# Kernel optimization log

Measured on AMD Instinct MI355X. Metric: run time of the kernel, lower is better.

## Reference

```python
import jax, jax.numpy as jnp
import numpy as np

NUM_CLASSES = 8
NUM_MAPS = 4
FEAT_C = 2048  # ResNet-50 layer4 channels
HW = 14        # spatial size (448/32)


def setup_inputs() -> dict:
    key = jax.random.key(0)
    k1, k2, k3, k4, k5 = jax.random.split(key, 5)
    B = 64
    x = jax.random.normal(k1, (B, FEAT_C, HW, HW), dtype=jnp.float32)
    down_w = jax.random.normal(k2, (NUM_CLASSES * NUM_MAPS, FEAT_C), dtype=jnp.float32) * 0.02
    down_b = jax.random.normal(k3, (NUM_CLASSES * NUM_MAPS,), dtype=jnp.float32) * 0.02
    fc_w = jax.random.normal(k4, (NUM_CLASSES, 2 * FEAT_C), dtype=jnp.float32) * 0.02
    fc_b = jax.random.normal(k5, (NUM_CLASSES,), dtype=jnp.float32) * 0.02
    return {"x": x, "down_w": down_w, "down_b": down_b, "fc_w": fc_w, "fc_b": fc_b}


def reference(x, down_w, down_b, fc_w, fc_b):
    B = x.shape[0]
    x_ori = x  # [B, 2048, 14, 14] (ResNet features output)
    # downconv: 1x1 conv 2048 -> num_classes*num_maps
    xc = jnp.einsum('bchw,oc->bohw', x_ori, down_w) + down_b[None, :, None, None]  # [B,32,14,14]
    # GMP over full 14x14 window -> [B, 32]
    gmp = jnp.max(xc, axis=(2, 3))
    # spatial_pooling = ClassWisePool(num_maps): mean over groups of num_maps channels
    scores = gmp.reshape(B, NUM_CLASSES, NUM_MAPS).mean(axis=2)  # [B, 8]
    x_out = jax.nn.log_softmax(scores, axis=1)  # first output
    # class-wise pool on the full conv map: [B,32,14,14] -> [B,8,14,14]
    xcp = xc.reshape(B, NUM_CLASSES, NUM_MAPS, HW, HW).mean(axis=2)
    # modulate each class map by its (log-softmax) score
    xcp = xcp * x_out[:, :, None, None]
    # spatial_pooling2 = ClassWisePool(num_classes): mean over 8 class channels -> [B,1,14,14]
    sal = xcp.mean(axis=1, keepdims=True)
    prod = sal * x_ori  # [B,2048,14,14] via broadcast (fused, no copies)
    cat = jnp.concatenate([x_ori, prod], axis=1)  # [B,4096,14,14]
    # GAP 14x14 -> [B,4096]
    gap = cat.mean(axis=(2, 3))
    logits2 = gap @ fc_w.T + fc_b  # [B,8]
    x_conv_out = jax.nn.log_softmax(logits2, axis=1)
    return (x_out, x_conv_out)
```

## Files before the change

kernel.cpp:

```cpp
#include <hip/hip_runtime.h>

#define NCLS 8
#define NMAPS 4
#define NCH 2048
#define HW 196
#define NB 64
#define NOUT 48
#define PF 8

__global__ void build_wct(const float* __restrict__ down_w,
                          const float* __restrict__ fc_w,
                          float* __restrict__ wct) {
    int i = blockIdx.x * 256 + threadIdx.x;
    if (i >= NCH * NOUT) return;
    int c = i / NOUT, o = i % NOUT;
    float v;
    if (o < 32)      v = down_w[o * NCH + c];
    else if (o < 40) v = fc_w[(o - 32) * (2 * NCH) + NCH + c];
    else             v = fc_w[(o - 40) * (2 * NCH) + c];
    wct[c * NOUT + o] = v;
}

__global__ __launch_bounds__(256) void conv48(const float* __restrict__ x,
                                              const float* __restrict__ wct,
                                              float* __restrict__ part,
                                              int cpc, int nchunk) {
    const int b = blockIdx.y;
    const int chunk = blockIdx.x;
    const int p = threadIdx.x;
    const int pp = (p < HW) ? p : (HW - 1);

    float acc[NOUT];
#pragma unroll
    for (int o = 0; o < NOUT; ++o) acc[o] = 0.f;

    const float* xb = x + ((size_t)b * NCH + (size_t)chunk * cpc) * HW + pp;
    const float* wb = wct + (size_t)chunk * cpc * NOUT;

    float xv[PF];
#pragma unroll
    for (int i = 0; i < PF; ++i) xv[i] = xb[i * HW];

    int c0 = 0;
    for (; c0 + 2 * PF <= cpc; c0 += PF) {
        float xn[PF];
#pragma unroll
        for (int i = 0; i < PF; ++i) xn[i] = xb[(c0 + PF + i) * HW];
#pragma unroll
        for (int i = 0; i < PF; ++i) {
            const float* w = wb + (c0 + i) * NOUT;
#pragma unroll
            for (int o = 0; o < NOUT; ++o)
                acc[o] = fmaf(w[o], xv[i], acc[o]);
        }
#pragma unroll
        for (int i = 0; i < PF; ++i) xv[i] = xn[i];
        __asm__ volatile("" ::: "memory");
    }
#pragma unroll
    for (int i = 0; i < PF; ++i) {
        const float* w = wb + (c0 + i) * NOUT;
#pragma unroll
        for (int o = 0; o < NOUT; ++o)
            acc[o] = fmaf(w[o], xv[i], acc[o]);
    }

    if (p < HW) {
        float* dst = part + ((size_t)(b * nchunk + chunk) * NOUT) * HW + p;
#pragma unroll
        for (int o = 0; o < NOUT; ++o) dst[o * HW] = acc[o];
    }
}

__global__ __launch_bounds__(256) void reduce_part(const float* __restrict__ part,
                                                   float* __restrict__ T,
                                                   int nchunk) {
    int idx = blockIdx.x * 256 + threadIdx.x;
    if (idx >= NB * NOUT * HW) return;
    int b = idx / (NOUT * HW);
    int rem = idx - b * NOUT * HW;
    const float* src = part + (size_t)b * nchunk * NOUT * HW + rem;
    float s = 0.f;
    for (int ch = 0; ch < nchunk; ++ch)
        s += src[(size_t)ch * NOUT * HW];
    T[idx] = s;
}

__global__ __launch_bounds__(256) void finish(const float* __restrict__ T,
                                              const float* __restrict__ down_b,
                                              const float* __restrict__ fc_b,
                                              float* __restrict__ out) {
    const int b = blockIdx.x;
    const int tid = threadIdx.x;
    __shared__ float Ts[NOUT * HW];
    __shared__ float gmpS[32];
    __shared__ float scoreS[8];
    __shared__ float xoS[8];
    __shared__ float salS[HW];
    __shared__ float logitS[8];

    {
        const float4* src = (const float4*)(T + (size_t)b * NOUT * HW);
        float4* dst = (float4*)Ts;
        for (int i = tid; i < NOUT * HW / 4; i += 256) dst[i] = src[i];
    }
    __syncthreads();

    if (tid < 32) {
        float m = -1e30f;
        for (int p = 0; p < HW; ++p) m = fmaxf(m, Ts[tid * HW + p]);
        gmpS[tid] = m + down_b[tid];
    }
    __syncthreads();

    if (tid < 8)
        scoreS[tid] = 0.25f * (gmpS[4 * tid] + gmpS[4 * tid + 1] +
                               gmpS[4 * tid + 2] + gmpS[4 * tid + 3]);
    __syncthreads();

    if (tid < 8) {
        float m = -1e30f;
        for (int k = 0; k < 8; ++k) m = fmaxf(m, scoreS[k]);
        float se = 0.f;
        for (int k = 0; k < 8; ++k) se += expf(scoreS[k] - m);
        float xo = scoreS[tid] - m - logf(se);
        xoS[tid] = xo;
        out[b * 8 + tid] = xo;
    }
    __syncthreads();

    if (tid < HW) {
        float s = 0.f;
#pragma unroll
        for (int k = 0; k < 8; ++k) {
            float bs = down_b[4 * k] + down_b[4 * k + 1] +
                       down_b[4 * k + 2] + down_b[4 * k + 3];
            float rs = Ts[(4 * k) * HW + tid] + Ts[(4 * k + 1) * HW + tid] +
                       Ts[(4 * k + 2) * HW + tid] + Ts[(4 * k + 3) * HW + tid] + bs;
            s += xoS[k] * rs;
        }
        salS[tid] = s * (1.f / 32.f);
    }
    __syncthreads();

    if (tid < 8) {
        float t1 = 0.f, t2 = 0.f;
        for (int p = 0; p < HW; ++p) {
            t1 += Ts[(40 + tid) * HW + p];
            t2 += salS[p] * Ts[(32 + tid) * HW + p];
        }
        logitS[tid] = (t1 + t2) * (1.f / 196.f) + fc_b[tid];
    }
    __syncthreads();

    if (tid < 8) {
        float m = -1e30f;
        for (int k = 0; k < 8; ++k) m = fmaxf(m, logitS[k]);
        float se = 0.f;
        for (int k = 0; k < 8; ++k) se += expf(logitS[k] - m);
        out[NB * 8 + b * 8 + tid] = logitS[tid] - m - logf(se);
    }
}

extern "C" void kernel_launch(void* const* d_in, const int* in_sizes, int n_in,
                              void* d_out, int out_size, void* d_ws, size_t ws_size,
                              hipStream_t stream) {
    const float* x      = (const float*)d_in[0];
    const float* down_w = (const float*)d_in[1];
    const float* down_b = (const float*)d_in[2];
    const float* fc_w   = (const float*)d_in[3];
    const float* fc_b   = (const float*)d_in[4];
    float* out = (float*)d_out;

    float* wct  = (float*)d_ws;
    float* T    = wct + NCH * NOUT;
    float* part = T + NB * NOUT * HW;

    size_t base_bytes = ((size_t)NCH * NOUT + (size_t)NB * NOUT * HW) * 4;
    int nchunk = 16;
    if (ws_size < base_bytes + (size_t)NB * 16 * NOUT * HW * 4) nchunk = 8;
    int cpc = NCH / nchunk;

    build_wct<<<(NCH * NOUT + 255) / 256, 256, 0, stream>>>(down_w, fc_w, wct);
    conv48<<<dim3(nchunk, NB), 256, 0, stream>>>(x, wct, part, cpc, nchunk);
    reduce_part<<<(NB * NOUT * HW + 255) / 256, 256, 0, stream>>>(part, T, nchunk);
    finish<<<NB, 256, 0, stream>>>(T, down_b, fc_b, out);
}
```

Before: 205.1 us.

## Split conv outputs into three groups and fold partial reduction into finish

The conv kernel now computes 16 of the 48 output channels per block, with three blocks per channel chunk, cutting accumulator registers to allow more waves per CU. The number of channel chunks drops from 16 to 8, and the separate reduce_part kernel is removed: finish sums the per-chunk partials itself while loading into shared memory. build_wct remaps threads so reads of the source weights are contiguous. In exchange, each x slice is read three times, relying on cache reuse between the sibling blocks that run close together.

```diff
diff --git a/kernel.cpp b/kernel.cpp
--- a/kernel.cpp
+++ b/kernel.cpp
@@ -6,6 +6,8 @@
 #define HW 196
 #define NB 64
 #define NOUT 48
+#define OG 3
+#define OPG 16
 #define PF 8
 
 __global__ void build_wct(const float* __restrict__ down_w,
@@ -13,7 +15,8 @@
                           float* __restrict__ wct) {
     int i = blockIdx.x * 256 + threadIdx.x;
     if (i >= NCH * NOUT) return;
-    int c = i / NOUT, o = i % NOUT;
+    int o = i >> 11;
+    int c = i & (NCH - 1);
     float v;
     if (o < 32)      v = down_w[o * NCH + c];
     else if (o < 40) v = fc_w[(o - 32) * (2 * NCH) + NCH + c];
@@ -26,16 +29,17 @@
                                               float* __restrict__ part,
                                               int cpc, int nchunk) {
     const int b = blockIdx.y;
-    const int chunk = blockIdx.x;
+    const int chunk = blockIdx.x / OG;
+    const int og = blockIdx.x - chunk * OG;
     const int p = threadIdx.x;
     const int pp = (p < HW) ? p : (HW - 1);
 
-    float acc[NOUT];
+    float acc[OPG];
 #pragma unroll
-    for (int o = 0; o < NOUT; ++o) acc[o] = 0.f;
+    for (int o = 0; o < OPG; ++o) acc[o] = 0.f;
 
     const float* xb = x + ((size_t)b * NCH + (size_t)chunk * cpc) * HW + pp;
-    const float* wb = wct + (size_t)chunk * cpc * NOUT;
+    const float* wb = wct + (size_t)chunk * cpc * NOUT + og * OPG;
 
     float xv[PF];
 #pragma unroll
@@ -50,7 +54,7 @@
         for (int i = 0; i < PF; ++i) {
             const float* w = wb + (c0 + i) * NOUT;
 #pragma unroll
-            for (int o = 0; o < NOUT; ++o)
+            for (int o = 0; o < OPG; ++o)
                 acc[o] = fmaf(w[o], xv[i], acc[o]);
         }
 #pragma unroll
@@ -61,35 +65,22 @@
     for (int i = 0; i < PF; ++i) {
         const float* w = wb + (c0 + i) * NOUT;
 #pragma unroll
-        for (int o = 0; o < NOUT; ++o)
+        for (int o = 0; o < OPG; ++o)
             acc[o] = fmaf(w[o], xv[i], acc[o]);
     }
 
     if (p < HW) {
-        float* dst = part + ((size_t)(b * nchunk + chunk) * NOUT) * HW + p;
+        float* dst = part + ((size_t)(b * nchunk + chunk) * NOUT + og * OPG) * HW + p;
 #pragma unroll
-        for (int o = 0; o < NOUT; ++o) dst[o * HW] = acc[o];
+        for (int o = 0; o < OPG; ++o) dst[o * HW] = acc[o];
     }
 }
 
-__global__ __launch_bounds__(256) void reduce_part(const float* __restrict__ part,
-                                                   float* __restrict__ T,
-                                                   int nchunk) {
-    int idx = blockIdx.x * 256 + threadIdx.x;
-    if (idx >= NB * NOUT * HW) return;
-    int b = idx / (NOUT * HW);
-    int rem = idx - b * NOUT * HW;
-    const float* src = part + (size_t)b * nchunk * NOUT * HW + rem;
-    float s = 0.f;
-    for (int ch = 0; ch < nchunk; ++ch)
-        s += src[(size_t)ch * NOUT * HW];
-    T[idx] = s;
-}
-
-__global__ __launch_bounds__(256) void finish(const float* __restrict__ T,
+__global__ __launch_bounds__(256) void finish(const float* __restrict__ part,
                                               const float* __restrict__ down_b,
                                               const float* __restrict__ fc_b,
-                                              float* __restrict__ out) {
+                                              float* __restrict__ out,
+                                              int nchunk) {
     const int b = blockIdx.x;
     const int tid = threadIdx.x;
     __shared__ float Ts[NOUT * HW];
@@ -100,9 +91,17 @@
     __shared__ float logitS[8];
 
     {
-        const float4* src = (const float4*)(T + (size_t)b * NOUT * HW);
+        const float4* src = (const float4*)(part + (size_t)b * nchunk * NOUT * HW);
         float4* dst = (float4*)Ts;
-        for (int i = tid; i < NOUT * HW / 4; i += 256) dst[i] = src[i];
+        const int n4 = NOUT * HW / 4;
+        for (int i = tid; i < n4; i += 256) {
+            float4 s = src[i];
+            for (int ch = 1; ch < nchunk; ++ch) {
+                float4 v = src[(size_t)ch * n4 + i];
+                s.x += v.x; s.y += v.y; s.z += v.z; s.w += v.w;
+            }
+            dst[i] = s;
+        }
     }
     __syncthreads();
 
@@ -173,16 +172,14 @@
     float* out = (float*)d_out;
 
     float* wct  = (float*)d_ws;
-    float* T    = wct + NCH * NOUT;
-    float* part = T + NB * NOUT * HW;
+    float* part = wct + NCH * NOUT;
 
-    size_t base_bytes = ((size_t)NCH * NOUT + (size_t)NB * NOUT * HW) * 4;
-    int nchunk = 16;
-    if (ws_size < base_bytes + (size_t)NB * 16 * NOUT * HW * 4) nchunk = 8;
+    size_t base_bytes = (size_t)NCH * NOUT * 4;
+    int nchunk = 8;
+    if (ws_size < base_bytes + (size_t)NB * 8 * NOUT * HW * 4) nchunk = 4;
     int cpc = NCH / nchunk;
 
     build_wct<<<(NCH * NOUT + 255) / 256, 256, 0, stream>>>(down_w, fc_w, wct);
-    conv48<<<dim3(nchunk, NB), 256, 0, stream>>>(x, wct, part, cpc, nchunk);
-    reduce_part<<<(NB * NOUT * HW + 255) / 256, 256, 0, stream>>>(part, T, nchunk);
-    finish<<<NB, 256, 0, stream>>>(T, down_b, fc_b, out);
+    conv48<<<dim3(nchunk * OG, NB), 256, 0, stream>>>(x, wct, part, cpc, nchunk);
+    finish<<<NB, 256, 0, stream>>>(part, down_b, fc_b, out, nchunk);
 }
```

After: 202.6 us. About the same (-1.2%).

## Replace FP32 FMA channel conv with bf16 MFMA 16x16x32 kernel

Applied to the files above, without the earlier changes.

The 1x1 conv plus the fused fc projections, a 48-output GEMM over 2048 channels, now runs on bf16 matrix cores instead of scalar FP32 FMAs. Weights are pre-packed into MFMA A-fragment layout in bf16. Each wave converts strided x loads to bf16 on the fly and issues three MFMAs per 16-pixel tile. This cuts ALU work but lowers precision to bf16 inputs. The chunk count is fixed at 16, removing the workspace-size fallback.

```diff
diff --git a/kernel.cpp b/kernel.cpp
--- a/kernel.cpp
+++ b/kernel.cpp
@@ -1,87 +1,120 @@
 #include <hip/hip_runtime.h>
 
-#define NCLS 8
-#define NMAPS 4
 #define NCH 2048
 #define HW 196
 #define NB 64
 #define NOUT 48
-#define PF 8
-
-__global__ void build_wct(const float* __restrict__ down_w,
-                          const float* __restrict__ fc_w,
-                          float* __restrict__ wct) {
-    int i = blockIdx.x * 256 + threadIdx.x;
-    if (i >= NCH * NOUT) return;
-    int c = i / NOUT, o = i % NOUT;
-    float v;
-    if (o < 32)      v = down_w[o * NCH + c];
-    else if (o < 40) v = fc_w[(o - 32) * (2 * NCH) + NCH + c];
-    else             v = fc_w[(o - 40) * (2 * NCH) + c];
-    wct[c * NOUT + o] = v;
-}
-
-__global__ __launch_bounds__(256) void conv48(const float* __restrict__ x,
-                                              const float* __restrict__ wct,
-                                              float* __restrict__ part,
-                                              int cpc, int nchunk) {
+#define NCHUNK 16
+#define CPC (NCH / NCHUNK)
+#define KSTEPS (CPC / 32)
+#define KGTOT (NCH / 32)
+#define NT 13
+#define MT 3
+
+typedef __attribute__((ext_vector_type(8))) short bf16x8;
+typedef __attribute__((ext_vector_type(4))) float f32x4;
+
+__device__ __forceinline__ short f2bf(float f) {
+    unsigned int u = __float_as_uint(f);
+    u = u + 0x7fffu + ((u >> 16) & 1u);
+    return (short)(u >> 16);
+}
+
+__global__ void build_afrag(const float* __restrict__ down_w,
+                            const float* __restrict__ fc_w,
+                            bf16x8* __restrict__ afrag) {
+    int t = blockIdx.x * 256 + threadIdx.x;
+    if (t >= KGTOT * MT * 64) return;
+    int lane = t & 63;
+    int frag = t >> 6;
+    int mt = frag % MT;
+    int kg = frag / MT;
+    int o = mt * 16 + (lane & 15);
+    int cbase = kg * 32 + (lane >> 4) * 8;
+    bf16x8 v;
+#pragma unroll
+    for (int j = 0; j < 8; ++j) {
+        int c = cbase + j;
+        float w;
+        if (o < 32)      w = down_w[o * NCH + c];
+        else if (o < 40) w = fc_w[(o - 32) * (2 * NCH) + NCH + c];
+        else             w = fc_w[(o - 40) * (2 * NCH) + c];
+        v[j] = f2bf(w);
+    }
+    afrag[frag * 64 + lane] = v;
+}
+
+__global__ __launch_bounds__(256, 4) void conv_mfma(const float* __restrict__ x,
+                                                    const bf16x8* __restrict__ afrag,
+                                                    float* __restrict__ part) {
+    const int chunk = blockIdx.x;
     const int b = blockIdx.y;
-    const int chunk = blockIdx.x;
-    const int p = threadIdx.x;
-    const int pp = (p < HW) ? p : (HW - 1);
-
-    float acc[NOUT];
-#pragma unroll
-    for (int o = 0; o < NOUT; ++o) acc[o] = 0.f;
-
-    const float* xb = x + ((size_t)b * NCH + (size_t)chunk * cpc) * HW + pp;
-    const float* wb = wct + (size_t)chunk * cpc * NOUT;
-
-    float xv[PF];
-#pragma unroll
-    for (int i = 0; i < PF; ++i) xv[i] = xb[i * HW];
-
-    int c0 = 0;
-    for (; c0 + 2 * PF <= cpc; c0 += PF) {
-        float xn[PF];
-#pragma unroll
-        for (int i = 0; i < PF; ++i) xn[i] = xb[(c0 + PF + i) * HW];
-#pragma unroll
-        for (int i = 0; i < PF; ++i) {
-            const float* w = wb + (c0 + i) * NOUT;
-#pragma unroll
-            for (int o = 0; o < NOUT; ++o)
-                acc[o] = fmaf(w[o], xv[i], acc[o]);
-        }
-#pragma unroll
-        for (int i = 0; i < PF; ++i) xv[i] = xn[i];
-        __asm__ volatile("" ::: "memory");
-    }
-#pragma unroll
-    for (int i = 0; i < PF; ++i) {
-        const float* w = wb + (c0 + i) * NOUT;
-#pragma unroll
-        for (int o = 0; o < NOUT; ++o)
-            acc[o] = fmaf(w[o], xv[i], acc[o]);
-    }
-
-    if (p < HW) {
-        float* dst = part + ((size_t)(b * nchunk + chunk) * NOUT) * HW + p;
-#pragma unroll
-        for (int o = 0; o < NOUT; ++o) dst[o * HW] = acc[o];
+    const int wave = threadIdx.x >> 6;
+    const int lane = threadIdx.x & 63;
+    const int nsub = lane & 15;
+    const int kq = lane >> 4;
+
+    f32x4 acc[4][MT];
+#pragma unroll
+    for (int i = 0; i < 4; ++i)
+#pragma unroll
+        for (int m = 0; m < MT; ++m)
+            acc[i][m] = (f32x4){0.f, 0.f, 0.f, 0.f};
+
+    int pidx[4];
+#pragma unroll
+    for (int i = 0; i < 4; ++i) {
+        int p = (wave + 4 * i) * 16 + nsub;
+        pidx[i] = (p < HW) ? p : (HW - 1);
+    }
+
+    const float* xb = x + ((size_t)b * NCH + (size_t)chunk * CPC) * HW;
+
+    for (int ks = 0; ks < KSTEPS; ++ks) {
+        const int kg = chunk * KSTEPS + ks;
+        bf16x8 a0 = afrag[(kg * MT + 0) * 64 + lane];
+        bf16x8 a1 = afrag[(kg * MT + 1) * 64 + lane];
+        bf16x8 a2 = afrag[(kg * MT + 2) * 64 + lane];
+        const float* xk = xb + (ks * 32 + kq * 8) * HW;
+#pragma unroll
+        for (int i = 0; i < 4; ++i) {
+            float f[8];
+#pragma unroll
+            for (int j = 0; j < 8; ++j) f[j] = xk[j * HW + pidx[i]];
+            bf16x8 bv;
+#pragma unroll
+            for (int j = 0; j < 8; ++j) bv[j] = f2bf(f[j]);
+            acc[i][0] = __builtin_amdgcn_mfma_f32_16x16x32_bf16(a0, bv, acc[i][0], 0, 0, 0);
+            acc[i][1] = __builtin_amdgcn_mfma_f32_16x16x32_bf16(a1, bv, acc[i][1], 0, 0, 0);
+            acc[i][2] = __builtin_amdgcn_mfma_f32_16x16x32_bf16(a2, bv, acc[i][2], 0, 0, 0);
+        }
+    }
+
+    float* dst = part + ((size_t)(b * NCHUNK + chunk) * NOUT) * HW;
+#pragma unroll
+    for (int i = 0; i < 4; ++i) {
+        int nt = wave + 4 * i;
+        int p = nt * 16 + nsub;
+        if (nt < NT && p < HW) {
+#pragma unroll
+            for (int m = 0; m < MT; ++m)
+#pragma unroll
+                for (int r = 0; r < 4; ++r)
+                    dst[(m * 16 + kq * 4 + r) * HW + p] = acc[i][m][r];
+        }
     }
 }
 
 __global__ __launch_bounds__(256) void reduce_part(const float* __restrict__ part,
-                                                   float* __restrict__ T,
-                                                   int nchunk) {
+                                                   float* __restrict__ T) {
     int idx = blockIdx.x * 256 + threadIdx.x;
     if (idx >= NB * NOUT * HW) return;
     int b = idx / (NOUT * HW);
-    int rem = idx - b * NOUT * HW;
-    const float* src = part + (size_t)b * nchunk * NOUT * HW + rem;
+    int rem = idx - b * (NOUT * HW);
+    const float* src = part + (size_t)b * NCHUNK * NOUT * HW + rem;
     float s = 0.f;
-    for (int ch = 0; ch < nchunk; ++ch)
+#pragma unroll
+    for (int ch = 0; ch < NCHUNK; ++ch)
         s += src[(size_t)ch * NOUT * HW];
     T[idx] = s;
 }
@@ -172,17 +205,12 @@
     const float* fc_b   = (const float*)d_in[4];
     float* out = (float*)d_out;
 
-    float* wct  = (float*)d_ws;
-    float* T    = wct + NCH * NOUT;
-    float* part = T + NB * NOUT * HW;
-
-    size_t base_bytes = ((size_t)NCH * NOUT + (size_t)NB * NOUT * HW) * 4;
-    int nchunk = 16;
-    if (ws_size < base_bytes + (size_t)NB * 16 * NOUT * HW * 4) nchunk = 8;
-    int cpc = NCH / nchunk;
-
-    build_wct<<<(NCH * NOUT + 255) / 256, 256, 0, stream>>>(down_w, fc_w, wct);
-    conv48<<<dim3(nchunk, NB), 256, 0, stream>>>(x, wct, part, cpc, nchunk);
-    reduce_part<<<(NB * NOUT * HW + 255) / 256, 256, 0, stream>>>(part, T, nchunk);
+    bf16x8* afrag = (bf16x8*)d_ws;
+    float* T    = (float*)((char*)d_ws + (size_t)KGTOT * MT * 64 * 16);
+    float* part = T + (size_t)NB * NOUT * HW;
+
+    build_afrag<<<(KGTOT * MT * 64 + 255) / 256, 256, 0, stream>>>(down_w, fc_w, afrag);
+    conv_mfma<<<dim3(NCHUNK, NB), 256, 0, stream>>>(x, afrag, part);
+    reduce_part<<<(NB * NOUT * HW + 255) / 256, 256, 0, stream>>>(part, T);
     finish<<<NB, 256, 0, stream>>>(T, down_b, fc_b, out);
 }
```

New measurement: 202.0 us. Within noise of the previous version (-1.5%).
